# Optimization experiments

Hardware: AMD Instinct MI355X
Metric: run time of the kernel (lower is better)

The kernel has to match this reference:

```python
import jax, jax.numpy as jnp
import numpy as np

B, D, H = 131072, 128, 64  # batch, input_dim (down_ch), output_dim


def _lstm(x, h, c, w_ih, w_hh, b):
    # torch nn.LSTMCell math; gate order i, f, g, o
    gates = x @ w_ih.T + h @ w_hh.T + b
    i, f, g, o = jnp.split(gates, 4, axis=-1)
    c2 = jax.nn.sigmoid(f) * c + jax.nn.sigmoid(i) * jnp.tanh(g)
    h2 = jax.nn.sigmoid(o) * jnp.tanh(c2)
    return h2, c2


def _lstm0(x, w_ih, b):
    # LSTMCell with zero initial (h, c): h-term and f*c term vanish
    gates = x @ w_ih.T + b
    i, f, g, o = jnp.split(gates, 4, axis=-1)
    c2 = jax.nn.sigmoid(i) * jnp.tanh(g)
    h2 = jax.nn.sigmoid(o) * jnp.tanh(c2)
    return h2, c2


def _trans(x, w, stride):
    # trans(): Conv1d(1,1,k=3,stride,pad=1,bias=False) + softmax(dim=-1)
    # x: [N, W], w: [1, 1, 3]
    y = jax.lax.conv_general_dilated(x[:, None, :], w, (stride,), [(1, 1)],
                                     dimension_numbers=('NCH', 'OIH', 'NCH'))
    return jax.nn.softmax(y[:, 0, :], axis=-1)


def _forward(spec, fw_ih1, fw_hh1, fb1, fw_ih2, fw_hh2, fb2, fw_ih3, fw_hh3, fb3,
             fw_ih4, fw_hh4, fb4, bw_ih1, bw_hh1, bb1, bw_ih2, bw_hh2, bb2,
             bw_ih3, bw_hh3, bb3, bw_ih4, bw_hh4, bb4,
             ft12h, ft12c, ft23h, ft23c, ft34h,
             bt43h, bt43c, bt32h, bt32c, bt21h, bt21c):
    b = spec.shape[0]
    # multi-scale chunking of spec: x2=[b,2,64], x3=[b,4,32], x4=[b,8,16]
    x2 = spec.reshape(b, 2, D // 2)
    x3 = spec.reshape(b, 4, D // 4)
    x4 = spec.reshape(b, 8, D // 8)

    # ---- fwd_LSTM (short memory): coarse -> fine, trans stride 2 ----
    # every cell call uses a state taken from the previous scale's backup, so
    # all steps at a scale are independent -> fully vectorized over steps.
    h1, c1 = _lstm0(spec, fw_ih1, fb1)                                      # [b,64]
    hb = _trans(h1, ft12h, 2)                                               # [b,32]
    cb = _trans(c1, ft12c, 2)
    h2, c2 = _lstm(x2, hb[:, None, :], cb[:, None, :], fw_ih2, fw_hh2, fb2)  # [b,2,32]
    hb2 = _trans(h2.reshape(b * 2, 32), ft23h, 2).reshape(b, 2, 16)
    cb2 = _trans(c2.reshape(b * 2, 32), ft23c, 2).reshape(b, 2, 16)
    h3, c3 = _lstm(x3, jnp.repeat(hb2, 2, axis=1), jnp.repeat(cb2, 2, axis=1),
                   fw_ih3, fw_hh3, fb3)                                     # [b,4,16]
    hb3 = _trans(h3.reshape(b * 4, 16), ft34h, 2).reshape(b, 4, 8)
    cb3 = _trans(c3.reshape(b * 4, 16), ft34h, 2).reshape(b, 4, 8)  # original bug: trans3_4h reused for cx
    h4, _ = _lstm(x4, jnp.repeat(hb3, 2, axis=1), jnp.repeat(cb3, 2, axis=1),
                  fw_ih4, fw_hh4, fb4)                                      # [b,8,8]
    out_fwd = h4.reshape(b, 64)

    # ---- bwd_LSTM (long memory): fine -> coarse, trans stride 1 over pairs ----
    h4b, c4b = _lstm0(x4, bw_ih4, bb4)                                      # [b,8,8] (zero state each step)
    # pairs of consecutive steps concatenated along features == reshape(b,4,16)
    hb4 = _trans(h4b.reshape(b * 4, 16), bt43h, 1).reshape(b, 4, 16)
    cb4 = _trans(c4b.reshape(b * 4, 16), bt43c, 1).reshape(b, 4, 16)
    h3b, c3b = _lstm(x3, hb4, cb4, bw_ih3, bw_hh3, bb3)                     # [b,4,16]
    hb3b = _trans(h3b.reshape(b * 2, 32), bt32h, 1).reshape(b, 2, 32)
    cb3b = _trans(c3b.reshape(b * 2, 32), bt32c, 1).reshape(b, 2, 32)
    h2b, c2b = _lstm(x2, hb3b, cb3b, bw_ih2, bw_hh2, bb2)                   # [b,2,32]
    hb1b = _trans(h2b.reshape(b, 64), bt21h, 1)                             # [b,64]
    cb1b = _trans(c2b.reshape(b, 64), bt21c, 1)
    _, c1b = _lstm(spec, hb1b, cb1b, bw_ih1, bw_hh1, bb1)                   # [b,64]

    return jnp.concatenate([out_fwd, c1b], axis=-1)                         # [b,128]


def setup_inputs() -> dict:
    key = jax.random.key(0)
    ks = iter(jax.random.split(key, 64))

    def nrm(shape, s=0.08):
        return (jax.random.normal(next(ks), shape) * s).astype(jnp.float32)

    inp = {"spec": jax.random.normal(next(ks), (B, D), dtype=jnp.float32)}
    dims = [(D, H), (D // 2, H // 2), (D // 4, H // 4), (D // 8, H // 8)]
    for pre in ("f", "b"):
        for idx, (di, dh) in enumerate(dims, 1):
            inp[f"{pre}w_ih{idx}"] = nrm((4 * dh, di))
            inp[f"{pre}w_hh{idx}"] = nrm((4 * dh, dh))
            inp[f"{pre}b{idx}"] = nrm((4 * dh,))
    for name in ("ft12h", "ft12c", "ft23h", "ft23c", "ft34h",
                 "bt43h", "bt43c", "bt32h", "bt32c", "bt21h", "bt21c"):
        inp[name] = nrm((1, 1, 3), 0.5)
    return inp


def reference(spec, fw_ih1, fw_hh1, fb1, fw_ih2, fw_hh2, fb2, fw_ih3, fw_hh3, fb3,
              fw_ih4, fw_hh4, fb4, bw_ih1, bw_hh1, bb1, bw_ih2, bw_hh2, bb2,
              bw_ih3, bw_hh3, bb3, bw_ih4, bw_hh4, bb4,
              ft12h, ft12c, ft23h, ft23c, ft34h,
              bt43h, bt43c, bt32h, bt32c, bt21h, bt21c):
    return _forward(spec, fw_ih1, fw_hh1, fb1, fw_ih2, fw_hh2, fb2, fw_ih3, fw_hh3,
                    fb3, fw_ih4, fw_hh4, fb4, bw_ih1, bw_hh1, bb1, bw_ih2, bw_hh2,
                    bb2, bw_ih3, bw_hh3, bb3, bw_ih4, bw_hh4, bb4,
                    ft12h, ft12c, ft23h, ft23c, ft34h,
                    bt43h, bt43c, bt32h, bt32c, bt21h, bt21c)
```

## Files before the change

kernel.cpp:

```cpp
#include <hip/hip_runtime.h>

typedef __attribute__((ext_vector_type(4))) float f32x4;
typedef __attribute__((ext_vector_type(8))) short short8;

#define DEV __device__ __forceinline__

DEV float fastrcp(float x){ return __builtin_amdgcn_rcpf(x); }
DEV float exp2r(float x){ return __builtin_amdgcn_exp2f(x); }

DEV float lstm_c(float gi, float gf, float gg, float cb){
  float v = exp2r(gi*-1.44269504f);
  float u = exp2r(gf*-1.44269504f);
  float w = exp2r(gg*2.88539008f);
  float pv = 1.f+v, pu = 1.f+u, pw = 1.f+w;
  float pvw = pv*pw;
  return (cb*pvw + (w-1.f)*pu) * fastrcp(pu*pvw);
}
DEV float lstm_h(float go, float c){
  float x = exp2r(go*-1.44269504f);
  float y = exp2r(c*2.88539008f);
  return (y-1.f)*fastrcp((1.f+x)*(1.f+y));
}
DEV float lstm0_c(float gi, float gg){
  float v = exp2r(gi*-1.44269504f);
  float w = exp2r(gg*2.88539008f);
  return (w-1.f)*fastrcp((1.f+v)*(1.f+w));
}

DEV unsigned cvtpk(float lo, float hi){ unsigned r; asm("v_cvt_pk_bf16_f32 %0, %1, %2" : "=v"(r) : "v"(lo), "v"(hi)); return r; }
DEV unsigned short f2bf(float f){ return (unsigned short)cvtpk(f,f); }
DEV float bf2f(unsigned short h){ return __uint_as_float(((unsigned)h)<<16); }
DEV unsigned pack2(float a, float b){ return cvtpk(a,b); }

DEV int gmask(int f){ return ((f&1)<<5) | (f&2) | ((f&4)<<2); }
DEV void stBF(char* A, int f, int b, float v){ *(unsigned short*)(A + (((f<<6) + (b ^ gmask(f)))<<1)) = f2bf(v); }
DEV void stBFpair(char* A, int f, int b, float v0, float v1){
  *(unsigned*)(A + (((f<<6) + (b ^ gmask(f)))<<1)) = cvtpk(v0, v1);
}
DEV float ldBF(const char* A, int f, int b){ return bf2f(*(const unsigned short*)(A + (((f<<6) + (b ^ gmask(f)))<<1))); }
DEV float2 ldBF2(const char* A, int f, int b){
  unsigned u = *(const unsigned*)(A + (((f<<6) + (b ^ gmask(f)))<<1));
  return make_float2(__uint_as_float(u<<16), __uint_as_float(u & 0xffff0000u));
}

DEV short8 frag(const char* p){ return *(const short8*)p; }
DEV short8 gfrag(const char* p){ return *(const short8*)p; }
DEV f32x4 MF(short8 a, short8 b, f32x4 c){ return __builtin_amdgcn_mfma_f32_16x16x32_bf16(a,b,c,0,0,0); }

struct P {
  const float *spec;
  const float *fw_ih1,*fw_hh1,*fb1,*fw_ih2,*fw_hh2,*fb2,*fw_ih3,*fw_hh3,*fb3,*fw_ih4,*fw_hh4,*fb4;
  const float *bw_ih1,*bw_hh1,*bb1,*bw_ih2,*bw_hh2,*bb2,*bw_ih3,*bw_hh3,*bb3,*bw_ih4,*bw_hh4,*bb4;
  const float *ft12h,*ft12c,*ft23h,*ft23c,*ft34h,*bt43h,*bt43c,*bt32h,*bt32c,*bt21h,*bt21c;
  float *out;
};

#define OF1 0
#define OF2 48
#define OF3 72
#define OF4 80
#define OB4 86
#define OB3 90
#define OB2 98
#define OB1 122
#define BLOBB (194*1024)

__global__ __launch_bounds__(256) void dsgsf_prep(P p, char* blob){
  int s = blockIdx.x;
  if (s == 3 || s == 4){
    bool isF = (s == 3);
    const float* wih = isF ? p.fw_ih4 : p.bw_ih4;
    const float* whh = p.fw_hh4;
    int nslot = isF ? 6 : 4;
    int off   = isF ? OF4 : OB4;
    for (int n = threadIdx.x; n < nslot*64; n += 256){
      int st = n>>6, lx = n&63;
      int R = lx&15, half = R>>3, feat = R&7;
      int k0 = ((lx>>4)<<3);
      unsigned dw[4];
      #pragma unroll
      for (int q=0;q<4;++q){
        float a=0.f, bv=0.f;
        int ka=k0+2*q, kb=ka+1;
        if (isF){
          if (st < 4){
            int pp = st>>1, t = st&1;
            int gi = t*2 + half;
            int src = gi*8 + feat, base = pp*16;
            if (ka>=base && ka<base+16) a  = wih[src*16 + (ka-base)];
            if (kb>=base && kb<base+16) bv = wih[src*16 + (kb-base)];
          } else {
            int t = st-4; int gi = t*2 + half; int src = gi*8 + feat;
            if (ka<8) a  = whh[src*8+ka];
            if (kb<8) bv = whh[src*8+kb];
          }
        } else {
          int pp = st>>1, t = st&1;
          int gi = (t==0) ? (half? 2:0) : (half? -1:3);
          if (gi >= 0){
            int src = gi*8 + feat, base = pp*16;
            if (ka>=base && ka<base+16) a  = wih[src*16 + (ka-base)];
            if (kb>=base && kb<base+16) bv = wih[src*16 + (kb-base)];
          }
        }
        dw[q] = pack2(a,bv);
      }
      *(uint4*)(blob + (size_t)(off+st)*1024 + lx*16) = make_uint4(dw[0],dw[1],dw[2],dw[3]);
    }
    return;
  }
  const float* wih=nullptr; const float* whh=nullptr;
  int H=0,NG=0,Kx=0,KXT=0,Kh=0,KT=0,NT=0,off=0,o0=0,o1=1,o2=2,o3=3;
  switch(s){
    case 0: wih=p.fw_ih1;               H=64;NG=3;Kx=128;KXT=4;Kh=0; KT=4;NT=12;off=OF1;o1=2;o2=3; break;
    case 1: wih=p.fw_ih2; whh=p.fw_hh2; H=32;NG=4;Kx=64; KXT=2;Kh=32;KT=3;NT=8; off=OF2; break;
    case 2: wih=p.fw_ih3; whh=p.fw_hh3; H=16;NG=4;Kx=32; KXT=1;Kh=16;KT=2;NT=4; off=OF3; break;
    case 5: wih=p.bw_ih3; whh=p.bw_hh3; H=16;NG=4;Kx=32; KXT=1;Kh=16;KT=2;NT=4; off=OB3; break;
    case 6: wih=p.bw_ih2; whh=p.bw_hh2; H=32;NG=4;Kx=64; KXT=2;Kh=32;KT=3;NT=8; off=OB2; break;
    default:wih=p.bw_ih1; whh=p.bw_hh1; H=64;NG=3;Kx=128;KXT=4;Kh=64;KT=6;NT=12;off=OB1; break;
  }
  int total = KT*NT*64;
  for (int n = threadIdx.x; n < total; n += 256){
    int kt = n/(NT*64); int rem = n - kt*NT*64; int nt = rem>>6; int lx = rem&63;
    int R = nt*16 + (lx&15);
    int gi = R / H; int feat = R - gi*H;
    int og = (gi==0)? o0 : (gi==1)? o1 : (gi==2)? o2 : o3;
    int src = og*H + feat;
    int k0 = kt*32 + ((lx>>4)<<3);
    unsigned dw[4];
    #pragma unroll
    for (int q=0;q<4;++q){
      float a=0.f, b=0.f;
      int ka=k0+2*q, kb=ka+1;
      if (gi < NG){
        if (ka < Kx) a = wih[(size_t)src*Kx + ka];
        else { int kh = ka - KXT*32; if (kh>=0 && kh<Kh) a = whh[(size_t)src*Kh + kh]; }
        if (kb < Kx) b = wih[(size_t)src*Kx + kb];
        else { int kh = kb - KXT*32; if (kh>=0 && kh<Kh) b = whh[(size_t)src*Kh + kh]; }
      }
      dw[q] = pack2(a,b);
    }
    *(uint4*)(blob + (size_t)off*1024 + (size_t)(kt*NT + nt)*1024 + lx*16) =
        make_uint4(dw[0],dw[1],dw[2],dw[3]);
  }
}

template<int NG,int NFT,int KT, class AF>
DEV void gemm_reg(f32x4 (&acc)[2][NG], const char* bstage, int nf, int mtp, int l, AF af){
  constexpr int NT = NG*NFT;
  #pragma unroll
  for (int kt=0; kt<KT; ++kt){
    short8 a0 = af(kt, mtp*2);
    short8 a1 = af(kt, mtp*2+1);
    #pragma unroll
    for (int g=0; g<NG; ++g){
      short8 bf = gfrag(bstage + (size_t)(kt*NT + g*NFT + nf)*1024 + l*16);
      acc[0][g] = MF(a0, bf, acc[0][g]);
      acc[1][g] = MF(a1, bf, acc[1][g]);
    }
  }
}

template<int NG>
DEV void binit(f32x4 (&acc)[2][NG], const float* bias, int H, int feat,
               int o0, int o1, int o2, int o3){
  int og[4] = {o0,o1,o2,o3};
  #pragma unroll
  for (int g=0; g<NG; ++g){
    float bv = bias[og[g]*H + feat];
    f32x4 v = {bv,bv,bv,bv};
    acc[0][g]=v; acc[1][g]=v;
  }
}

DEV void pw4(const f32x4 (&acc)[2][4], char* AH, char* AC, const char* BC,
             int arow, int cbrow, int mtp, int l){
  #pragma unroll
  for (int mtI=0;mtI<2;++mtI){
    float hv[4], cv[4];
    int bb = (mtp*2+mtI)*16 + ((l>>4)<<2);
    float2 cb01 = ldBF2(BC, cbrow, bb), cb23 = ldBF2(BC, cbrow, bb+2);
    float cbv[4] = {cb01.x, cb01.y, cb23.x, cb23.y};
    #pragma unroll
    for (int r=0;r<4;++r){
      cv[r] = lstm_c(acc[mtI][0][r], acc[mtI][1][r], acc[mtI][2][r], cbv[r]);
      hv[r] = lstm_h(acc[mtI][3][r], cv[r]);
    }
    stBFpair(AH, arow, bb,   hv[0], hv[1]);
    stBFpair(AH, arow, bb+2, hv[2], hv[3]);
    stBFpair(AC, arow, bb,   cv[0], cv[1]);
    stBFpair(AC, arow, bb+2, cv[2], cv[3]);
  }
}

template<int L,int NO>
DEV void convE1(const char* Ain, int row0, const float* tw, int o0, int b,
                float (&y)[NO], float& s){
  float w0=tw[0]*1.44269504f, w1=tw[1]*1.44269504f, w2=tw[2]*1.44269504f;
  s = 0.f;
  float prev = (o0 >= 1) ? ldBF(Ain, row0+o0-1, b) : 0.f;
  float cur  = ldBF(Ain, row0+o0, b);
  #pragma unroll
  for (int j=0;j<NO;++j){
    int c = o0 + j;
    float nxt;
    if (j < NO-1) nxt = ldBF(Ain, row0+c+1, b);
    else          nxt = (o0+NO < L) ? ldBF(Ain, row0+c+1, b) : 0.f;
    float v = w0*prev + w1*cur + w2*nxt;
    y[j] = exp2r(v); s += y[j];
    prev = cur; cur = nxt;
  }
}
template<int L,int NO>
DEV void convE2(const char* Ain, int row0, const float* tw, int o0, int b,
                float (&y)[NO], float& s){
  float w0=tw[0]*1.44269504f, w1=tw[1]*1.44269504f, w2=tw[2]*1.44269504f;
  s = 0.f;
  float left = (o0 >= 1) ? ldBF(Ain, row0+2*o0-1, b) : 0.f;
  #pragma unroll
  for (int j=0;j<NO;++j){
    int c = 2*(o0+j);
    float mid = ldBF(Ain, row0+c,   b);
    float rgt = ldBF(Ain, row0+c+1, b);
    float v = w0*left + w1*mid + w2*rgt;
    y[j] = exp2r(v); s += y[j];
    left = rgt;
  }
}
template<int SZ,int NO>
DEV void wrTF(char* TFb, int subBase, int o0, int b, const float (&y)[NO], float inv){
  #pragma unroll
  for (int g8=0; g8<NO/8; ++g8){
    int oo = o0 + g8*8, fl = oo&31;
    char* base = TFb + (size_t)((subBase+(oo>>5))*4+(b>>4))*SZ + ((b&15)+16*(fl>>3))*16;
    unsigned d0=cvtpk(y[g8*8+0]*inv,y[g8*8+1]*inv), d1=cvtpk(y[g8*8+2]*inv,y[g8*8+3]*inv);
    unsigned d2=cvtpk(y[g8*8+4]*inv,y[g8*8+5]*inv), d3=cvtpk(y[g8*8+6]*inv,y[g8*8+7]*inv);
    *(uint4*)base = make_uint4(d0,d1,d2,d3);
  }
}
template<int NO>
DEV void wrBC(char* BCb, int row0, int b, const float (&y)[NO], float inv){
  #pragma unroll
  for (int j=0;j<NO;++j) stBF(BCb, row0+j, b, y[j]*inv);
}

__global__ __launch_bounds__(512, 4) void dsgsf_main(P p, const char* blob){
  __shared__ __align__(16) char SM[51200];
  char* XP = SM;
  char* AH = SM + 16384;
  char* AC = SM + 24576;
  char* BC = SM + 32768;
  char* TF = SM + 40960;
  float* PSm = (float*)(SM + 49152);

  const int tid = threadIdx.x;
  const int l   = tid & 63;
  const int wu  = __builtin_amdgcn_readfirstlane(tid >> 6);
  const int mtp = wu & 1, z = wu >> 1;
  const long b0 = (long)blockIdx.x * 64;

  #pragma unroll
  for (int it=0; it<2; ++it){
    int n = it*512 + tid; int slot = n>>6, lx = n&63;
    int kc = slot>>2, mt = slot&3;
    const float* sp = p.spec + (b0 + mt*16 + (lx&15))*128 + kc*32 + ((lx>>4)<<3);
    float4 v0 = *(const float4*)sp; float4 v1 = *(const float4*)(sp+4);
    unsigned d0=cvtpk(v0.x,v0.y), d1=cvtpk(v0.z,v0.w);
    unsigned d2=cvtpk(v1.x,v1.y), d3=cvtpk(v1.z,v1.w);
    *(uint4*)(XP + (size_t)slot*1024 + lx*16) = make_uint4(d0,d1,d2,d3);
  }
  __syncthreads();

  {
    f32x4 acc[2][3];
    int feat = z*16 + (l&15);
    binit<3>(acc, p.fb1, 64, feat, 0,2,3,0);
    auto af = [&](int kt, int mt){ return frag(XP + (size_t)((kt<<2)+mt)*1024 + l*16); };
    gemm_reg<3,4,4>(acc, blob + (size_t)OF1*1024, z, mtp, l, af);
    #pragma unroll
    for (int mtI=0;mtI<2;++mtI){
      float hv[4], cv[4];
      int bb = (mtp*2+mtI)*16 + ((l>>4)<<2);
      #pragma unroll
      for (int r=0;r<4;++r){
        cv[r] = lstm0_c(acc[mtI][0][r], acc[mtI][1][r]);
        hv[r] = lstm_h(acc[mtI][2][r], cv[r]);
      }
      stBFpair(AH, feat, bb,   hv[0], hv[1]);
      stBFpair(AH, feat, bb+2, hv[2], hv[3]);
      stBFpair(AC, feat, bb,   cv[0], cv[1]);
      stBFpair(AC, feat, bb+2, cv[2], cv[3]);
    }
  }
  __syncthreads();

  {
    float y[8], s;
    if (wu<4) convE2<64,8>(AH, 0, p.ft12h, wu*8, l, y, s);
    else      convE2<64,8>(AC, 0, p.ft12c, (wu-4)*8, l, y, s);
    PSm[wu*64+l] = s;
    __syncthreads();
    float tot = (wu<4) ? PSm[0*64+l]+PSm[1*64+l]+PSm[2*64+l]+PSm[3*64+l]
                       : PSm[4*64+l]+PSm[5*64+l]+PSm[6*64+l]+PSm[7*64+l];
    float inv = fastrcp(tot);
    if (wu<4) wrTF<1024,8>(TF, 0, wu*8, l, y, inv);
    else      wrBC<8>(BC, (wu-4)*8, l, y, inv);
  }
  __syncthreads();

  {
    f32x4 acc[2][4];
    int step = z>>1, nf = z&1;
    int feat = nf*16 + (l&15);
    binit<4>(acc, p.fb2, 32, feat, 0,1,2,3);
    auto af = [&](int kt, int mt){
      return (kt<2) ? frag(XP + (size_t)(((2*step+kt)<<2)+mt)*1024 + l*16)
                    : frag(TF + (size_t)mt*1024 + l*16); };
    gemm_reg<4,2,3>(acc, blob + (size_t)OF2*1024, nf, mtp, l, af);
    pw4(acc, AH, AC, BC, step*32+feat, feat, mtp, l);
  }
  __syncthreads();

  {
    float y[8], s; int v=wu&3, st=v>>1, ch=v&1;
    if (wu<4) convE2<32,8>(AH, st*32, p.ft23h, ch*8, l, y, s);
    else      convE2<32,8>(AC, st*32, p.ft23c, ch*8, l, y, s);
    PSm[wu*64+l] = s;
    __syncthreads();
    int base = (wu&4) | (st<<1);
    float inv = fastrcp(PSm[base*64+l] + PSm[(base|1)*64+l]);
    if (wu<4) wrTF<512,8>(TF, st, ch*8, l, y, inv);
    else      wrBC<8>(BC, st*16+ch*8, l, y, inv);
  }
  __syncthreads();

  {
    f32x4 acc[2][4];
    int s = z, feat = l&15;
    binit<4>(acc, p.fb3, 16, feat, 0,1,2,3);
    auto af = [&](int kt, int mt){
      return (kt==0) ? frag(XP + (size_t)((s<<2)+mt)*1024 + l*16)
                     : frag(TF + (size_t)(((s>>1)<<2)+mt)*512 + (l&31)*16); };
    gemm_reg<4,1,2>(acc, blob + (size_t)OF3*1024, 0, mtp, l, af);
    pw4(acc, AH, AC, BC, s*16+feat, (s>>1)*16+feat, mtp, l);
  }
  __syncthreads();

  {
    float y[8], s;
    if (wu<4){ convE2<16,8>(AH, wu*16, p.ft34h, 0, l, y, s);
               wrTF<256,8>(TF, wu, 0, l, y, fastrcp(s)); }
    else     { convE2<16,8>(AC, (wu-4)*16, p.ft34h, 0, l, y, s);
               wrBC<8>(BC, (wu-4)*8, l, y, fastrcp(s)); }
  }
  __syncthreads();

  {
    f32x4 a4[2][2][2];
    float bv0 = p.fb4[l&15], bv1 = p.fb4[16+(l&15)];
    #pragma unroll
    for (int uu=0;uu<2;++uu)
      #pragma unroll
      for (int mtI=0;mtI<2;++mtI){ a4[uu][mtI][0]=f32x4{bv0,bv0,bv0,bv0}; a4[uu][mtI][1]=f32x4{bv1,bv1,bv1,bv1}; }
    const char* bs = blob + (size_t)OF4*1024;
    short8 A0 = frag(XP + (size_t)((z<<2)+mtp*2  )*1024 + l*16);
    short8 A1 = frag(XP + (size_t)((z<<2)+mtp*2+1)*1024 + l*16);
    short8 H0 = frag(TF + (size_t)((z<<2)+mtp*2  )*256 + (l&15)*16);
    short8 H1 = frag(TF + (size_t)((z<<2)+mtp*2+1)*256 + (l&15)*16);
    short8 bh0 = gfrag(bs + 4*1024 + l*16);
    short8 bh1 = gfrag(bs + 5*1024 + l*16);
    #pragma unroll
    for (int uu=0;uu<2;++uu){
      short8 bx0 = gfrag(bs + (uu*2+0)*1024 + l*16);
      short8 bx1 = gfrag(bs + (uu*2+1)*1024 + l*16);
      a4[uu][0][0]=MF(A0,bx0,a4[uu][0][0]); a4[uu][0][1]=MF(A0,bx1,a4[uu][0][1]);
      a4[uu][1][0]=MF(A1,bx0,a4[uu][1][0]); a4[uu][1][1]=MF(A1,bx1,a4[uu][1][1]);
      a4[uu][0][0]=MF(H0,bh0,a4[uu][0][0]); a4[uu][0][1]=MF(H0,bh1,a4[uu][0][1]);
      a4[uu][1][0]=MF(H1,bh0,a4[uu][1][0]); a4[uu][1][1]=MF(H1,bh1,a4[uu][1][1]);
    }
    const bool sel = (l&15) < 8;
    const int qe = l&7;
    const int u = z*2 + (sel ? 0 : 1);
    #pragma unroll
    for (int mtI=0;mtI<2;++mtI){
      int bb = (mtp*2+mtI)*16 + ((l>>4)<<2);
      float2 cb01 = ldBF2(BC, z*8+qe, bb), cb23 = ldBF2(BC, z*8+qe, bb+2);
      float cbv[4] = {cb01.x, cb01.y, cb23.x, cb23.y};
      #pragma unroll
      for (int r=0;r<4;++r){
        float s00 = __shfl_xor(a4[0][mtI][0][r],8), s10 = __shfl_xor(a4[1][mtI][0][r],8);
        float s01 = __shfl_xor(a4[0][mtI][1][r],8), s11 = __shfl_xor(a4[1][mtI][1][r],8);
        float iv = sel ? a4[0][mtI][0][r] : s10;
        float fv = sel ? s00 : a4[1][mtI][0][r];
        float gv = sel ? a4[0][mtI][1][r] : s11;
        float ov = sel ? s01 : a4[1][mtI][1][r];
        float c = lstm_c(iv, fv, gv, cbv[r]);
        float h = lstm_h(ov, c);
        p.out[(size_t)(b0+bb+r)*128 + u*8 + qe] = h;
      }
    }
  }

  {
    f32x4 a4[2][2][2];
    float bv0 = ((l&15)<8) ? p.bb4[l&15] : p.bb4[(l&15)+8];
    float bv1 = ((l&15)<8) ? p.bb4[24+(l&15)] : 0.f;
    #pragma unroll
    for (int uu=0;uu<2;++uu)
      #pragma unroll
      for (int mtI=0;mtI<2;++mtI){ a4[uu][mtI][0]=f32x4{bv0,bv0,bv0,bv0}; a4[uu][mtI][1]=f32x4{bv1,bv1,bv1,bv1}; }
    const char* bs = blob + (size_t)OB4*1024;
    short8 A0 = frag(XP + (size_t)((z<<2)+mtp*2  )*1024 + l*16);
    short8 A1 = frag(XP + (size_t)((z<<2)+mtp*2+1)*1024 + l*16);
    #pragma unroll
    for (int uu=0;uu<2;++uu){
      short8 bx0 = gfrag(bs + (uu*2+0)*1024 + l*16);
      short8 bx1 = gfrag(bs + (uu*2+1)*1024 + l*16);
      a4[uu][0][0]=MF(A0,bx0,a4[uu][0][0]); a4[uu][0][1]=MF(A0,bx1,a4[uu][0][1]);
      a4[uu][1][0]=MF(A1,bx0,a4[uu][1][0]); a4[uu][1][1]=MF(A1,bx1,a4[uu][1][1]);
    }
    const bool sel = (l&15) < 8;
    const int qe = l&7;
    const int u = z*2 + (sel ? 0 : 1);
    const int f = u*8 + qe;
    #pragma unroll
    for (int mtI=0;mtI<2;++mtI){
      float hv[4], cv[4];
      int bb = (mtp*2+mtI)*16 + ((l>>4)<<2);
      #pragma unroll
      for (int r=0;r<4;++r){
        float s0 = __shfl_xor(a4[0][mtI][0][r],8);
        float s1 = __shfl_xor(a4[1][mtI][0][r],8);
        float s2 = __shfl_xor(a4[1][mtI][1][r],8);
        float iv = sel ? a4[0][mtI][0][r] : s1;
        float gv = sel ? s0 : a4[1][mtI][0][r];
        float ov = sel ? a4[0][mtI][1][r] : s2;
        cv[r] = lstm0_c(iv, gv);
        hv[r] = lstm_h(ov, cv[r]);
      }
      stBFpair(AH, f, bb,   hv[0], hv[1]);
      stBFpair(AH, f, bb+2, hv[2], hv[3]);
      stBFpair(AC, f, bb,   cv[0], cv[1]);
      stBFpair(AC, f, bb+2, cv[2], cv[3]);
    }
  }
  __syncthreads();

  {
    float y[16], s;
    if (wu<4){ convE1<16,16>(AH, wu*16, p.bt43h, 0, l, y, s);
               wrTF<512,16>(TF, wu, 0, l, y, fastrcp(s)); }
    else     { convE1<16,16>(AC, (wu-4)*16, p.bt43c, 0, l, y, s);
               wrBC<16>(BC, (wu-4)*16, l, y, fastrcp(s)); }
  }
  __syncthreads();

  {
    f32x4 acc[2][4];
    int s = z, feat = l&15;
    binit<4>(acc, p.bb3, 16, feat, 0,1,2,3);
    auto af = [&](int kt, int mt){
      return (kt==0) ? frag(XP + (size_t)((s<<2)+mt)*1024 + l*16)
                     : frag(TF + (size_t)((s<<2)+mt)*512 + (l&31)*16); };
    gemm_reg<4,1,2>(acc, blob + (size_t)OB3*1024, 0, mtp, l, af);
    pw4(acc, AH, AC, BC, s*16+feat, s*16+feat, mtp, l);
  }
  __syncthreads();

  {
    float y[16], s; int v=wu&3, st=v>>1, ch=v&1;
    if (wu<4) convE1<32,16>(AH, st*32, p.bt32h, ch*16, l, y, s);
    else      convE1<32,16>(AC, st*32, p.bt32c, ch*16, l, y, s);
    PSm[wu*64+l] = s;
    __syncthreads();
    int base = (wu&4) | (st<<1);
    float inv = fastrcp(PSm[base*64+l] + PSm[(base|1)*64+l]);
    if (wu<4) wrTF<1024,16>(TF, st, ch*16, l, y, inv);
    else      wrBC<16>(BC, st*32+ch*16, l, y, inv);
  }
  __syncthreads();

  {
    f32x4 acc[2][4];
    int t2 = z>>1, nf = z&1;
    int feat = nf*16 + (l&15);
    binit<4>(acc, p.bb2, 32, feat, 0,1,2,3);
    auto af = [&](int kt, int mt){
      return (kt<2) ? frag(XP + (size_t)(((2*t2+kt)<<2)+mt)*1024 + l*16)
                    : frag(TF + (size_t)((t2<<2)+mt)*1024 + l*16); };
    gemm_reg<4,2,3>(acc, blob + (size_t)OB2*1024, nf, mtp, l, af);
    pw4(acc, AH, AC, BC, t2*32+feat, t2*32+feat, mtp, l);
  }
  __syncthreads();

  {
    float y[16], s;
    if (wu<4) convE1<64,16>(AH, 0, p.bt21h, wu*16, l, y, s);
    else      convE1<64,16>(AC, 0, p.bt21c, (wu-4)*16, l, y, s);
    PSm[wu*64+l] = s;
    __syncthreads();
    float tot = (wu<4) ? PSm[0*64+l]+PSm[1*64+l]+PSm[2*64+l]+PSm[3*64+l]
                       : PSm[4*64+l]+PSm[5*64+l]+PSm[6*64+l]+PSm[7*64+l];
    float inv = fastrcp(tot);
    if (wu<4) wrTF<1024,16>(TF, 0, wu*16, l, y, inv);
    else      wrBC<16>(BC, (wu-4)*16, l, y, inv);
  }
  __syncthreads();

  {
    f32x4 acc[2][3];
    int feat = z*16 + (l&15);
    binit<3>(acc, p.bb1, 64, feat, 0,1,2,0);
    auto af = [&](int kt, int mt){
      return (kt<4) ? frag(XP + (size_t)((kt<<2)+mt)*1024 + l*16)
                    : frag(TF + (size_t)(((kt-4)<<2)+mt)*1024 + l*16); };
    gemm_reg<3,4,6>(acc, blob + (size_t)OB1*1024, z, mtp, l, af);
    #pragma unroll
    for (int mtI=0;mtI<2;++mtI){
      int bb = (mtp*2+mtI)*16 + ((l>>4)<<2);
      float2 cb01 = ldBF2(BC, feat, bb), cb23 = ldBF2(BC, feat, bb+2);
      float cbv[4] = {cb01.x, cb01.y, cb23.x, cb23.y};
      #pragma unroll
      for (int r=0;r<4;++r){
        float c = lstm_c(acc[mtI][0][r], acc[mtI][1][r], acc[mtI][2][r], cbv[r]);
        p.out[(size_t)(b0+bb+r)*128 + 64 + feat] = c;
      }
    }
  }
}

extern "C" void kernel_launch(void* const* d_in, const int* in_sizes, int n_in,
                              void* d_out, int out_size, void* d_ws, size_t ws_size,
                              hipStream_t stream) {
  if (ws_size < (size_t)BLOBB) return;
  P p;
  p.spec   = (const float*)d_in[0];
  p.fw_ih1 = (const float*)d_in[1];  p.fw_hh1 = (const float*)d_in[2];  p.fb1 = (const float*)d_in[3];
  p.fw_ih2 = (const float*)d_in[4];  p.fw_hh2 = (const float*)d_in[5];  p.fb2 = (const float*)d_in[6];
  p.fw_ih3 = (const float*)d_in[7];  p.fw_hh3 = (const float*)d_in[8];  p.fb3 = (const float*)d_in[9];
  p.fw_ih4 = (const float*)d_in[10]; p.fw_hh4 = (const float*)d_in[11]; p.fb4 = (const float*)d_in[12];
  p.bw_ih1 = (const float*)d_in[13]; p.bw_hh1 = (const float*)d_in[14]; p.bb1 = (const float*)d_in[15];
  p.bw_ih2 = (const float*)d_in[16]; p.bw_hh2 = (const float*)d_in[17]; p.bb2 = (const float*)d_in[18];
  p.bw_ih3 = (const float*)d_in[19]; p.bw_hh3 = (const float*)d_in[20]; p.bb3 = (const float*)d_in[21];
  p.bw_ih4 = (const float*)d_in[22]; p.bw_hh4 = (const float*)d_in[23]; p.bb4 = (const float*)d_in[24];
  p.ft12h = (const float*)d_in[25]; p.ft12c = (const float*)d_in[26];
  p.ft23h = (const float*)d_in[27]; p.ft23c = (const float*)d_in[28];
  p.ft34h = (const float*)d_in[29];
  p.bt43h = (const float*)d_in[30]; p.bt43c = (const float*)d_in[31];
  p.bt32h = (const float*)d_in[32]; p.bt32c = (const float*)d_in[33];
  p.bt21h = (const float*)d_in[34]; p.bt21c = (const float*)d_in[35];
  p.out = (float*)d_out;

  char* blob = (char*)d_ws;
  hipLaunchKernelGGL(dsgsf_prep, dim3(8), dim3(256), 0, stream, p, blob);
  int Bn = in_sizes[0] / 128;
  hipLaunchKernelGGL(dsgsf_main, dim3(Bn/64), dim3(512), 0, stream, p, (const char*)blob);
}
```

Baseline: 145.4 us.

## Interleave forward and backward LSTM chains and keep spec fragments in registers

The forward and backward multi-scale LSTM chains now run interleaved within the same barrier phases. Each chain gets its own shared-memory buffers, so the number of __syncthreads phases drops and independent work from both chains can overlap. The spec input is also converted straight into bf16 MFMA A-fragments held in registers, which removes the LDS staging buffer, its barrier and the repeated LDS fragment reads. The cost is more shared memory per block (60KB) and more live registers (xf plus two chains' state), which may limit occupancy under launch_bounds(512,4).

```diff
diff --git a/kernel.cpp b/kernel.cpp
--- a/kernel.cpp
+++ b/kernel.cpp
@@ -2,6 +2,7 @@
 
 typedef __attribute__((ext_vector_type(4))) float f32x4;
 typedef __attribute__((ext_vector_type(8))) short short8;
+typedef __attribute__((ext_vector_type(4))) unsigned u32x4;
 
 #define DEV __device__ __forceinline__
 
@@ -146,12 +147,12 @@
 }
 
 template<int NG,int NFT,int KT, class AF>
-DEV void gemm_reg(f32x4 (&acc)[2][NG], const char* bstage, int nf, int mtp, int l, AF af){
+DEV void gemm_reg(f32x4 (&acc)[2][NG], const char* bstage, int nf, int l, AF af){
   constexpr int NT = NG*NFT;
   #pragma unroll
   for (int kt=0; kt<KT; ++kt){
-    short8 a0 = af(kt, mtp*2);
-    short8 a1 = af(kt, mtp*2+1);
+    short8 a0 = af(kt, 0);
+    short8 a1 = af(kt, 1);
     #pragma unroll
     for (int g=0; g<NG; ++g){
       short8 bf = gfrag(bstage + (size_t)(kt*NT + g*NFT + nf)*1024 + l*16);
@@ -245,13 +246,16 @@
 }
 
 __global__ __launch_bounds__(512, 4) void dsgsf_main(P p, const char* blob){
-  __shared__ __align__(16) char SM[51200];
-  char* XP = SM;
-  char* AH = SM + 16384;
-  char* AC = SM + 24576;
-  char* BC = SM + 32768;
-  char* TF = SM + 40960;
-  float* PSm = (float*)(SM + 49152);
+  __shared__ __align__(16) char SM[61440];
+  char* AHF = SM;
+  char* ACF = SM + 8192;
+  char* AHB = SM + 16384;
+  char* ACB = SM + 24576;
+  char* BCF = SM + 32768;
+  char* BCB = SM + 36864;
+  char* TFF = SM + 45056;
+  char* TFB = SM + 49152;
+  float* PSm = (float*)(SM + 57344);
 
   const int tid = threadIdx.x;
   const int l   = tid & 63;
@@ -259,24 +263,32 @@
   const int mtp = wu & 1, z = wu >> 1;
   const long b0 = (long)blockIdx.x * 64;
 
-  #pragma unroll
-  for (int it=0; it<2; ++it){
-    int n = it*512 + tid; int slot = n>>6, lx = n&63;
-    int kc = slot>>2, mt = slot&3;
-    const float* sp = p.spec + (b0 + mt*16 + (lx&15))*128 + kc*32 + ((lx>>4)<<3);
-    float4 v0 = *(const float4*)sp; float4 v1 = *(const float4*)(sp+4);
-    unsigned d0=cvtpk(v0.x,v0.y), d1=cvtpk(v0.z,v0.w);
-    unsigned d2=cvtpk(v1.x,v1.y), d3=cvtpk(v1.z,v1.w);
-    *(uint4*)(XP + (size_t)slot*1024 + lx*16) = make_uint4(d0,d1,d2,d3);
-  }
-  __syncthreads();
+  short8 xf[4][2];
+  {
+    const float* sp0 = p.spec + (b0 + mtp*32 + (l&15))*128 + ((l>>4)<<3);
+    #pragma unroll
+    for (int mtI=0;mtI<2;++mtI){
+      #pragma unroll
+      for (int kc=0;kc<4;++kc){
+        const float* sp = sp0 + mtI*16*128 + kc*32;
+        float4 v0 = *(const float4*)sp;
+        float4 v1 = *(const float4*)(sp+4);
+        xf[kc][mtI] = __builtin_bit_cast(short8,
+          (u32x4){cvtpk(v0.x,v0.y), cvtpk(v0.z,v0.w), cvtpk(v1.x,v1.y), cvtpk(v1.z,v1.w)});
+      }
+    }
+  }
+  auto xsel = [&](int kc, int mtI)->short8 {
+    switch(kc){ case 0: return xf[0][mtI]; case 1: return xf[1][mtI];
+                case 2: return xf[2][mtI]; default: return xf[3][mtI]; }
+  };
 
   {
     f32x4 acc[2][3];
     int feat = z*16 + (l&15);
     binit<3>(acc, p.fb1, 64, feat, 0,2,3,0);
-    auto af = [&](int kt, int mt){ return frag(XP + (size_t)((kt<<2)+mt)*1024 + l*16); };
-    gemm_reg<3,4,4>(acc, blob + (size_t)OF1*1024, z, mtp, l, af);
+    gemm_reg<3,4,4>(acc, blob + (size_t)OF1*1024, z, l,
+                    [&](int kt,int mtI){ return xf[kt][mtI]; });
     #pragma unroll
     for (int mtI=0;mtI<2;++mtI){
       float hv[4], cv[4];
@@ -286,25 +298,74 @@
         cv[r] = lstm0_c(acc[mtI][0][r], acc[mtI][1][r]);
         hv[r] = lstm_h(acc[mtI][2][r], cv[r]);
       }
-      stBFpair(AH, feat, bb,   hv[0], hv[1]);
-      stBFpair(AH, feat, bb+2, hv[2], hv[3]);
-      stBFpair(AC, feat, bb,   cv[0], cv[1]);
-      stBFpair(AC, feat, bb+2, cv[2], cv[3]);
+      stBFpair(AHF, feat, bb,   hv[0], hv[1]);
+      stBFpair(AHF, feat, bb+2, hv[2], hv[3]);
+      stBFpair(ACF, feat, bb,   cv[0], cv[1]);
+      stBFpair(ACF, feat, bb+2, cv[2], cv[3]);
+    }
+  }
+  {
+    f32x4 a4[2][2][2];
+    float bv0 = ((l&15)<8) ? p.bb4[l&15] : p.bb4[(l&15)+8];
+    float bv1 = ((l&15)<8) ? p.bb4[24+(l&15)] : 0.f;
+    #pragma unroll
+    for (int uu=0;uu<2;++uu)
+      #pragma unroll
+      for (int mtI=0;mtI<2;++mtI){ a4[uu][mtI][0]=f32x4{bv0,bv0,bv0,bv0}; a4[uu][mtI][1]=f32x4{bv1,bv1,bv1,bv1}; }
+    const char* bs = blob + (size_t)OB4*1024;
+    short8 A0 = xsel(z,0), A1 = xsel(z,1);
+    #pragma unroll
+    for (int uu=0;uu<2;++uu){
+      short8 bx0 = gfrag(bs + (uu*2+0)*1024 + l*16);
+      short8 bx1 = gfrag(bs + (uu*2+1)*1024 + l*16);
+      a4[uu][0][0]=MF(A0,bx0,a4[uu][0][0]); a4[uu][0][1]=MF(A0,bx1,a4[uu][0][1]);
+      a4[uu][1][0]=MF(A1,bx0,a4[uu][1][0]); a4[uu][1][1]=MF(A1,bx1,a4[uu][1][1]);
+    }
+    const bool sel = (l&15) < 8;
+    const int qe = l&7;
+    const int u = z*2 + (sel ? 0 : 1);
+    const int f = u*8 + qe;
+    #pragma unroll
+    for (int mtI=0;mtI<2;++mtI){
+      float hv[4], cv[4];
+      int bb = (mtp*2+mtI)*16 + ((l>>4)<<2);
+      #pragma unroll
+      for (int r=0;r<4;++r){
+        float s0 = __shfl_xor(a4[0][mtI][0][r],8);
+        float s1 = __shfl_xor(a4[1][mtI][0][r],8);
+        float s2 = __shfl_xor(a4[1][mtI][1][r],8);
+        float iv = sel ? a4[0][mtI][0][r] : s1;
+        float gv = sel ? s0 : a4[1][mtI][0][r];
+        float ov = sel ? a4[0][mtI][1][r] : s2;
+        cv[r] = lstm0_c(iv, gv);
+        hv[r] = lstm_h(ov, cv[r]);
+      }
+      stBFpair(AHB, f, bb,   hv[0], hv[1]);
+      stBFpair(AHB, f, bb+2, hv[2], hv[3]);
+      stBFpair(ACB, f, bb,   cv[0], cv[1]);
+      stBFpair(ACB, f, bb+2, cv[2], cv[3]);
     }
   }
   __syncthreads();
 
   {
-    float y[8], s;
-    if (wu<4) convE2<64,8>(AH, 0, p.ft12h, wu*8, l, y, s);
-    else      convE2<64,8>(AC, 0, p.ft12c, (wu-4)*8, l, y, s);
-    PSm[wu*64+l] = s;
+    float y12[8], s12;
+    if (wu<4) convE2<64,8>(AHF, 0, p.ft12h, wu*8, l, y12, s12);
+    else      convE2<64,8>(ACF, 0, p.ft12c, (wu-4)*8, l, y12, s12);
+    PSm[wu*64+l] = s12;
+    {
+      float y[16], s;
+      if (wu<4){ convE1<16,16>(AHB, wu*16, p.bt43h, 0, l, y, s);
+                 wrTF<512,16>(TFB, wu, 0, l, y, fastrcp(s)); }
+      else     { convE1<16,16>(ACB, (wu-4)*16, p.bt43c, 0, l, y, s);
+                 wrBC<16>(BCB, (wu-4)*16, l, y, fastrcp(s)); }
+    }
     __syncthreads();
     float tot = (wu<4) ? PSm[0*64+l]+PSm[1*64+l]+PSm[2*64+l]+PSm[3*64+l]
                        : PSm[4*64+l]+PSm[5*64+l]+PSm[6*64+l]+PSm[7*64+l];
     float inv = fastrcp(tot);
-    if (wu<4) wrTF<1024,8>(TF, 0, wu*8, l, y, inv);
-    else      wrBC<8>(BC, (wu-4)*8, l, y, inv);
+    if (wu<4) wrTF<1024,8>(TFF, 0, wu*8, l, y12, inv);
+    else      wrBC<8>(BCF, (wu-4)*8, l, y12, inv);
   }
   __syncthreads();
 
@@ -313,24 +374,42 @@
     int step = z>>1, nf = z&1;
     int feat = nf*16 + (l&15);
     binit<4>(acc, p.fb2, 32, feat, 0,1,2,3);
-    auto af = [&](int kt, int mt){
-      return (kt<2) ? frag(XP + (size_t)(((2*step+kt)<<2)+mt)*1024 + l*16)
-                    : frag(TF + (size_t)mt*1024 + l*16); };
-    gemm_reg<4,2,3>(acc, blob + (size_t)OF2*1024, nf, mtp, l, af);
-    pw4(acc, AH, AC, BC, step*32+feat, feat, mtp, l);
+    gemm_reg<4,2,3>(acc, blob + (size_t)OF2*1024, nf, l,
+      [&](int kt,int mtI){
+        return (kt<2) ? xsel(2*step+kt, mtI)
+                      : frag(TFF + (size_t)(mtp*2+mtI)*1024 + l*16); });
+    pw4(acc, AHF, ACF, BCF, step*32+feat, feat, mtp, l);
+  }
+  {
+    f32x4 acc[2][4];
+    int s = z, feat = l&15;
+    binit<4>(acc, p.bb3, 16, feat, 0,1,2,3);
+    gemm_reg<4,1,2>(acc, blob + (size_t)OB3*1024, 0, l,
+      [&](int kt,int mtI){
+        return (kt==0) ? xsel(s, mtI)
+                       : frag(TFB + (size_t)((s<<2)+mtp*2+mtI)*512 + (l&31)*16); });
+    pw4(acc, AHB, ACB, BCB, s*16+feat, s*16+feat, mtp, l);
   }
   __syncthreads();
 
   {
-    float y[8], s; int v=wu&3, st=v>>1, ch=v&1;
-    if (wu<4) convE2<32,8>(AH, st*32, p.ft23h, ch*8, l, y, s);
-    else      convE2<32,8>(AC, st*32, p.ft23c, ch*8, l, y, s);
-    PSm[wu*64+l] = s;
+    float y23[8], s23; int v23=wu&3, st23=v23>>1, ch23=v23&1;
+    if (wu<4) convE2<32,8>(AHF, st23*32, p.ft23h, ch23*8, l, y23, s23);
+    else      convE2<32,8>(ACF, st23*32, p.ft23c, ch23*8, l, y23, s23);
+    PSm[wu*64+l] = s23;
+    float y32[16], s32; int st32=(wu&3)>>1, ch32=wu&1;
+    if (wu<4) convE1<32,16>(AHB, st32*32, p.bt32h, ch32*16, l, y32, s32);
+    else      convE1<32,16>(ACB, st32*32, p.bt32c, ch32*16, l, y32, s32);
+    PSm[(8+wu)*64+l] = s32;
     __syncthreads();
-    int base = (wu&4) | (st<<1);
+    int base = (wu&4) | (st23<<1);
     float inv = fastrcp(PSm[base*64+l] + PSm[(base|1)*64+l]);
-    if (wu<4) wrTF<512,8>(TF, st, ch*8, l, y, inv);
-    else      wrBC<8>(BC, st*16+ch*8, l, y, inv);
+    if (wu<4) wrTF<512,8>(TFF, st23, ch23*8, l, y23, inv);
+    else      wrBC<8>(BCF, st23*16+ch23*8, l, y23, inv);
+    int base2 = 8 + ((wu&4) | (st32<<1));
+    float inv2 = fastrcp(PSm[base2*64+l] + PSm[(base2+1)*64+l]);
+    if (wu<4) wrTF<1024,16>(TFB, st32, ch32*16, l, y32, inv2);
+    else      wrBC<16>(BCB, st32*32+ch32*16, l, y32, inv2);
   }
   __syncthreads();
 
@@ -338,20 +417,43 @@
     f32x4 acc[2][4];
     int s = z, feat = l&15;
     binit<4>(acc, p.fb3, 16, feat, 0,1,2,3);
-    auto af = [&](int kt, int mt){
-      return (kt==0) ? frag(XP + (size_t)((s<<2)+mt)*1024 + l*16)
-                     : frag(TF + (size_t)(((s>>1)<<2)+mt)*512 + (l&31)*16); };
-    gemm_reg<4,1,2>(acc, blob + (size_t)OF3*1024, 0, mtp, l, af);
-    pw4(acc, AH, AC, BC, s*16+feat, (s>>1)*16+feat, mtp, l);
+    gemm_reg<4,1,2>(acc, blob + (size_t)OF3*1024, 0, l,
+      [&](int kt,int mtI){
+        return (kt==0) ? xsel(s, mtI)
+                       : frag(TFF + (size_t)(((s>>1)<<2)+mtp*2+mtI)*512 + (l&31)*16); });
+    pw4(acc, AHF, ACF, BCF, s*16+feat, (s>>1)*16+feat, mtp, l);
+  }
+  {
+    f32x4 acc[2][4];
+    int t2 = z>>1, nf = z&1;
+    int feat = nf*16 + (l&15);
+    binit<4>(acc, p.bb2, 32, feat, 0,1,2,3);
+    gemm_reg<4,2,3>(acc, blob + (size_t)OB2*1024, nf, l,
+      [&](int kt,int mtI){
+        return (kt<2) ? xsel(2*t2+kt, mtI)
+                      : frag(TFB + (size_t)((t2<<2)+mtp*2+mtI)*1024 + l*16); });
+    pw4(acc, AHB, ACB, BCB, t2*32+feat, t2*32+feat, mtp, l);
   }
   __syncthreads();
 
   {
-    float y[8], s;
-    if (wu<4){ convE2<16,8>(AH, wu*16, p.ft34h, 0, l, y, s);
-               wrTF<256,8>(TF, wu, 0, l, y, fastrcp(s)); }
-    else     { convE2<16,8>(AC, (wu-4)*16, p.ft34h, 0, l, y, s);
-               wrBC<8>(BC, (wu-4)*8, l, y, fastrcp(s)); }
+    {
+      float y[8], s;
+      if (wu<4){ convE2<16,8>(AHF, wu*16, p.ft34h, 0, l, y, s);
+                 wrTF<256,8>(TFF, wu, 0, l, y, fastrcp(s)); }
+      else     { convE2<16,8>(ACF, (wu-4)*16, p.ft34h, 0, l, y, s);
+                 wrBC<8>(BCF, (wu-4)*8, l, y, fastrcp(s)); }
+    }
+    float y21[16], s21;
+    if (wu<4) convE1<64,16>(AHB, 0, p.bt21h, wu*16, l, y21, s21);
+    else      convE1<64,16>(ACB, 0, p.bt21c, (wu-4)*16, l, y21, s21);
+    PSm[(8+wu)*64+l] = s21;
+    __syncthreads();
+    float tot = (wu<4) ? PSm[8*64+l]+PSm[9*64+l]+PSm[10*64+l]+PSm[11*64+l]
+                       : PSm[12*64+l]+PSm[13*64+l]+PSm[14*64+l]+PSm[15*64+l];
+    float inv = fastrcp(tot);
+    if (wu<4) wrTF<1024,16>(TFB, 0, wu*16, l, y21, inv);
+    else      wrBC<16>(BCB, (wu-4)*16, l, y21, inv);
   }
   __syncthreads();
 
@@ -363,10 +465,9 @@
       #pragma unroll
       for (int mtI=0;mtI<2;++mtI){ a4[uu][mtI][0]=f32x4{bv0,bv0,bv0,bv0}; a4[uu][mtI][1]=f32x4{bv1,bv1,bv1,bv1}; }
     const char* bs = blob + (size_t)OF4*1024;
-    short8 A0 = frag(XP + (size_t)((z<<2)+mtp*2  )*1024 + l*16);
-    short8 A1 = frag(XP + (size_t)((z<<2)+mtp*2+1)*1024 + l*16);
-    short8 H0 = frag(TF + (size_t)((z<<2)+mtp*2  )*256 + (l&15)*16);
-    short8 H1 = frag(TF + (size_t)((z<<2)+mtp*2+1)*256 + (l&15)*16);
+    short8 A0 = xsel(z,0), A1 = xsel(z,1);
+    short8 H0 = frag(TFF + (size_t)((z<<2)+mtp*2  )*256 + (l&15)*16);
+    short8 H1 = frag(TFF + (size_t)((z<<2)+mtp*2+1)*256 + (l&15)*16);
     short8 bh0 = gfrag(bs + 4*1024 + l*16);
     short8 bh1 = gfrag(bs + 5*1024 + l*16);
     #pragma unroll
@@ -384,7 +485,7 @@
     #pragma unroll
     for (int mtI=0;mtI<2;++mtI){
       int bb = (mtp*2+mtI)*16 + ((l>>4)<<2);
-      float2 cb01 = ldBF2(BC, z*8+qe, bb), cb23 = ldBF2(BC, z*8+qe, bb+2);
+      float2 cb01 = ldBF2(BCF, z*8+qe, bb), cb23 = ldBF2(BCF, z*8+qe, bb+2);
       float cbv[4] = {cb01.x, cb01.y, cb23.x, cb23.y};
       #pragma unroll
       for (int r=0;r<4;++r){
@@ -400,125 +501,18 @@
       }
     }
   }
-
-  {
-    f32x4 a4[2][2][2];
-    float bv0 = ((l&15)<8) ? p.bb4[l&15] : p.bb4[(l&15)+8];
-    float bv1 = ((l&15)<8) ? p.bb4[24+(l&15)] : 0.f;
-    #pragma unroll
-    for (int uu=0;uu<2;++uu)
-      #pragma unroll
-      for (int mtI=0;mtI<2;++mtI){ a4[uu][mtI][0]=f32x4{bv0,bv0,bv0,bv0}; a4[uu][mtI][1]=f32x4{bv1,bv1,bv1,bv1}; }
-    const char* bs = blob + (size_t)OB4*1024;
-    short8 A0 = frag(XP + (size_t)((z<<2)+mtp*2  )*1024 + l*16);
-    short8 A1 = frag(XP + (size_t)((z<<2)+mtp*2+1)*1024 + l*16);
-    #pragma unroll
-    for (int uu=0;uu<2;++uu){
-      short8 bx0 = gfrag(bs + (uu*2+0)*1024 + l*16);
-      short8 bx1 = gfrag(bs + (uu*2+1)*1024 + l*16);
-      a4[uu][0][0]=MF(A0,bx0,a4[uu][0][0]); a4[uu][0][1]=MF(A0,bx1,a4[uu][0][1]);
-      a4[uu][1][0]=MF(A1,bx0,a4[uu][1][0]); a4[uu][1][1]=MF(A1,bx1,a4[uu][1][1]);
-    }
-    const bool sel = (l&15) < 8;
-    const int qe = l&7;
-    const int u = z*2 + (sel ? 0 : 1);
-    const int f = u*8 + qe;
-    #pragma unroll
-    for (int mtI=0;mtI<2;++mtI){
-      float hv[4], cv[4];
-      int bb = (mtp*2+mtI)*16 + ((l>>4)<<2);
-      #pragma unroll
-      for (int r=0;r<4;++r){
-        float s0 = __shfl_xor(a4[0][mtI][0][r],8);
-        float s1 = __shfl_xor(a4[1][mtI][0][r],8);
-        float s2 = __shfl_xor(a4[1][mtI][1][r],8);
-        float iv = sel ? a4[0][mtI][0][r] : s1;
-        float gv = sel ? s0 : a4[1][mtI][0][r];
-        float ov = sel ? a4[0][mtI][1][r] : s2;
-        cv[r] = lstm0_c(iv, gv);
-        hv[r] = lstm_h(ov, cv[r]);
-      }
-      stBFpair(AH, f, bb,   hv[0], hv[1]);
-      stBFpair(AH, f, bb+2, hv[2], hv[3]);
-      stBFpair(AC, f, bb,   cv[0], cv[1]);
-      stBFpair(AC, f, bb+2, cv[2], cv[3]);
-    }
-  }
-  __syncthreads();
-
-  {
-    float y[16], s;
-    if (wu<4){ convE1<16,16>(AH, wu*16, p.bt43h, 0, l, y, s);
-               wrTF<512,16>(TF, wu, 0, l, y, fastrcp(s)); }
-    else     { convE1<16,16>(AC, (wu-4)*16, p.bt43c, 0, l, y, s);
-               wrBC<16>(BC, (wu-4)*16, l, y, fastrcp(s)); }
-  }
-  __syncthreads();
-
-  {
-    f32x4 acc[2][4];
-    int s = z, feat = l&15;
-    binit<4>(acc, p.bb3, 16, feat, 0,1,2,3);
-    auto af = [&](int kt, int mt){
-      return (kt==0) ? frag(XP + (size_t)((s<<2)+mt)*1024 + l*16)
-                     : frag(TF + (size_t)((s<<2)+mt)*512 + (l&31)*16); };
-    gemm_reg<4,1,2>(acc, blob + (size_t)OB3*1024, 0, mtp, l, af);
-    pw4(acc, AH, AC, BC, s*16+feat, s*16+feat, mtp, l);
-  }
-  __syncthreads();
-
-  {
-    float y[16], s; int v=wu&3, st=v>>1, ch=v&1;
-    if (wu<4) convE1<32,16>(AH, st*32, p.bt32h, ch*16, l, y, s);
-    else      convE1<32,16>(AC, st*32, p.bt32c, ch*16, l, y, s);
-    PSm[wu*64+l] = s;
-    __syncthreads();
-    int base = (wu&4) | (st<<1);
-    float inv = fastrcp(PSm[base*64+l] + PSm[(base|1)*64+l]);
-    if (wu<4) wrTF<1024,16>(TF, st, ch*16, l, y, inv);
-    else      wrBC<16>(BC, st*32+ch*16, l, y, inv);
-  }
-  __syncthreads();
-
-  {
-    f32x4 acc[2][4];
-    int t2 = z>>1, nf = z&1;
-    int feat = nf*16 + (l&15);
-    binit<4>(acc, p.bb2, 32, feat, 0,1,2,3);
-    auto af = [&](int kt, int mt){
-      return (kt<2) ? frag(XP + (size_t)(((2*t2+kt)<<2)+mt)*1024 + l*16)
-                    : frag(TF + (size_t)((t2<<2)+mt)*1024 + l*16); };
-    gemm_reg<4,2,3>(acc, blob + (size_t)OB2*1024, nf, mtp, l, af);
-    pw4(acc, AH, AC, BC, t2*32+feat, t2*32+feat, mtp, l);
-  }
-  __syncthreads();
-
-  {
-    float y[16], s;
-    if (wu<4) convE1<64,16>(AH, 0, p.bt21h, wu*16, l, y, s);
-    else      convE1<64,16>(AC, 0, p.bt21c, (wu-4)*16, l, y, s);
-    PSm[wu*64+l] = s;
-    __syncthreads();
-    float tot = (wu<4) ? PSm[0*64+l]+PSm[1*64+l]+PSm[2*64+l]+PSm[3*64+l]
-                       : PSm[4*64+l]+PSm[5*64+l]+PSm[6*64+l]+PSm[7*64+l];
-    float inv = fastrcp(tot);
-    if (wu<4) wrTF<1024,16>(TF, 0, wu*16, l, y, inv);
-    else      wrBC<16>(BC, (wu-4)*16, l, y, inv);
-  }
-  __syncthreads();
-
   {
     f32x4 acc[2][3];
     int feat = z*16 + (l&15);
     binit<3>(acc, p.bb1, 64, feat, 0,1,2,0);
-    auto af = [&](int kt, int mt){
-      return (kt<4) ? frag(XP + (size_t)((kt<<2)+mt)*1024 + l*16)
-                    : frag(TF + (size_t)(((kt-4)<<2)+mt)*1024 + l*16); };
-    gemm_reg<3,4,6>(acc, blob + (size_t)OB1*1024, z, mtp, l, af);
+    gemm_reg<3,4,6>(acc, blob + (size_t)OB1*1024, z, l,
+      [&](int kt,int mtI){
+        return (kt<4) ? xf[kt][mtI]
+                      : frag(TFB + (size_t)(((kt-4)<<2)+mtp*2+mtI)*1024 + l*16); });
     #pragma unroll
     for (int mtI=0;mtI<2;++mtI){
       int bb = (mtp*2+mtI)*16 + ((l>>4)<<2);
-      float2 cb01 = ldBF2(BC, feat, bb), cb23 = ldBF2(BC, feat, bb+2);
+      float2 cb01 = ldBF2(BCB, feat, bb), cb23 = ldBF2(BCB, feat, bb+2);
       float cbv[4] = {cb01.x, cb01.y, cb23.x, cb23.y};
       #pragma unroll
       for (int r=0;r<4;++r){
```

New measurement: 194.5 us. 1.34x slower.
